# Kernel optimization log

Hardware: AMD Instinct MI355X
Metric: run time of the kernel (lower is better)

## Reference

```python
import jax, jax.numpy as jnp
import numpy as np

HID = 128      # hidden_features
NF = 32        # noise_features
NPL = NF // 4  # noise features per layer
RES = 512      # noise grid resolution
N = 262144     # number of query points


def leaky_relu(x):
    return jax.nn.leaky_relu(x, negative_slope=0.01)


def sample_bilinear(image, coords):
    """image: [M, H, W]; coords: [..., M, 2] -> [..., M]"""
    M, Hn, Wn = image.shape
    x = coords[..., 0] - 0.5
    y = coords[..., 1] - 0.5
    x0f = jnp.floor(x)
    y0f = jnp.floor(y)
    xw = x - x0f
    yw = y - y0f
    x0 = x0f.astype(jnp.int32) % Wn
    x1 = (x0f.astype(jnp.int32) + 1) % Wn
    y0 = y0f.astype(jnp.int32) % Hn
    y1 = (y0f.astype(jnp.int32) + 1) % Hn
    f = jnp.arange(M)  # broadcasts against [..., M] index arrays
    i00 = image[f, y0, x0]
    i01 = image[f, y0, x1]
    i10 = image[f, y1, x0]
    i11 = image[f, y1, x1]
    i0 = i00 + (i01 - i00) * xw
    i1 = i10 + (i11 - i10) * xw
    return i0 + (i1 - i0) * yw


def setup_inputs() -> dict:
    key = jax.random.key(0)
    ks = jax.random.split(key, 12)
    noise = jax.random.normal(ks[0], (NF, RES, RES), dtype=jnp.float32)
    coords = jax.random.normal(ks[1], (N, 2), dtype=jnp.float32)
    # NoiseTransforms param: randn * 0.05 * 2**i per feature
    scale = 0.05 * (2.0 ** np.arange(NF)).astype(np.float32)
    transformations = jax.random.normal(ks[2], (NF, 2, 2), dtype=jnp.float32) * scale[:, None, None]
    input_vec = jnp.ones((HID,), dtype=jnp.float32)
    s_lin = 1.0 / np.sqrt(HID)
    s_noise = 1.0 / np.sqrt(NPL)
    lw = jax.random.uniform(ks[3], (4, HID, HID), jnp.float32, -s_lin, s_lin)
    lb = jax.random.uniform(ks[4], (4, HID), jnp.float32, -s_lin, s_lin)
    lnw = jax.random.uniform(ks[5], (4, HID, NPL), jnp.float32, -s_noise, s_noise)
    tw1 = jax.random.uniform(ks[6], (HID, HID), jnp.float32, -s_lin, s_lin)
    tb1 = jax.random.uniform(ks[7], (HID,), jnp.float32, -s_lin, s_lin)
    tw2 = jax.random.uniform(ks[8], (1, HID), jnp.float32, -s_lin, s_lin)
    tb2 = jax.random.uniform(ks[9], (1,), jnp.float32, -s_lin, s_lin)
    return {"noise": noise, "coords": coords, "transformations": transformations,
            "input_vec": input_vec, "lw": lw, "lb": lb, "lnw": lnw,
            "tw1": tw1, "tb1": tb1, "tw2": tw2, "tb2": tb2}


def reference(noise, coords, transformations, input_vec, lw, lb, lnw, tw1, tb1, tw2, tb2):
    # noise coords: [..., NF, 2]
    noise_coords = jnp.einsum('...n,Mmn->...Mm', coords, transformations)
    noise_values = sample_bilinear(noise, noise_coords)  # [..., NF]
    x = input_vec  # [HID], broadcasts up through layer adds
    for i in range(4):
        nv = noise_values[..., i * NPL:(i + 1) * NPL]
        x = leaky_relu(jnp.einsum('...h,oh->...o', x, lw[i]) + lb[i]
                       + jnp.einsum('...n,on->...o', nv, lnw[i]))
    h = leaky_relu(jnp.einsum('...h,oh->...o', x, tw1) + tb1)
    return jnp.einsum('...h,oh->...o', h, tw2) + tb2  # [..., 1]
```

## Files before the change

### kernel.cpp

```cpp
#include <hip/hip_runtime.h>

typedef _Float16 f16;
typedef f16 f16x4 __attribute__((ext_vector_type(4)));
typedef f16 f16x8 __attribute__((ext_vector_type(8)));
typedef float f32x4 __attribute__((ext_vector_type(4)));

#define RES 512
#define PTS 128
#define XS  136
#define AS  16


__global__ __launch_bounds__(256)
void pack_quad_k(const float* __restrict__ n, f16* __restrict__ q) {
    const int idx = blockIdx.x * 256 + threadIdx.x;
    const int qx = idx & 255, rest = idx >> 8;
    const int qy = rest & 255, m = rest >> 8;
    const float* src = n + ((size_t)m * 512 + 2 * qy) * 512 + 2 * qx;
    const float2 r0 = *(const float2*)(src);
    const float2 r1 = *(const float2*)(src + 512);
    f16x4 o; o[0]=(f16)r0.x; o[1]=(f16)r0.y; o[2]=(f16)r1.x; o[3]=(f16)r1.y;
    *(f16x4*)(q + (size_t)idx * 4) = o;
}

__global__ __launch_bounds__(256)
void pack_w_k(const float* __restrict__ lw,  const float* __restrict__ lnw,
              const float* __restrict__ lb,  const float* __restrict__ tw1,
              const float* __restrict__ tb1,
              f16* __restrict__ wf, f16* __restrict__ waugf) {
    const int g = blockIdx.x * 256 + threadIdx.x;
    if (g < 10240) {
        const int L = g >> 11, r = g & 2047;
        const int lane = r & 63, frag = r >> 6;
        const int q = lane >> 4, l15 = lane & 15;
        const int mt = frag >> 2, c = frag & 3;
        const float* src = ((L < 4) ? (lw + L * 16384) : tw1)
                           + (mt * 16 + l15) * 128 + c * 32 + q * 8;
        f16x8 h;
        #pragma unroll
        for (int j = 0; j < 8; ++j) h[j] = (f16)src[j];
        *(f16x8*)(wf + (size_t)g * 8) = h;
    } else {
        const int ga = g - 10240;
        const int L = ga >> 9, r = ga & 511;
        const int lane = r & 63, mt = r >> 6;
        const int q = lane >> 4, l15 = lane & 15;
        const int row = mt * 16 + l15;
        f16x8 h = {};
        if (q == 0 && L < 4) {
            const float* src = lnw + L * 1024 + row * 8;
            #pragma unroll
            for (int j = 0; j < 8; ++j) h[j] = (f16)src[j];
        }
        if (q == 1)
            h[0] = (f16)((L < 4) ? lb[L * 128 + row] : tb1[row]);
        *(f16x8*)(waugf + (size_t)ga * 8) = h;
    }
}

__device__ __forceinline__ float quad_tap(uint2 q, int sy, int sx) {
    unsigned w = sy ? q.y : q.x;
    w >>= (sx << 4);
    union { unsigned short u; f16 h; } cv; cv.u = (unsigned short)w;
    return (float)cv.h;
}

template <bool QUAD>
__global__ __launch_bounds__(256, 8)
void sample_kernel(const void* __restrict__ noise_v,
                   const float* __restrict__ coords,
                   const float* __restrict__ trans,
                   f16* __restrict__ nv_ws, const int Ntot)
{
    __shared__ float T_sh[128];
    const int t = threadIdx.x;
    if (t < 128) T_sh[t] = trans[t];
    __syncthreads();

    const int g = blockIdx.x & 7;
    const int p = (blockIdx.x >> 3) * 256 + t;

    int mk[4];
    if (g < 7) { mk[0] = g; mk[1] = g + 9; mk[2] = g + 17; mk[3] = g + 25; }
    else       { mk[0] = 7; mk[1] = 8;     mk[2] = 16;     mk[3] = 24;     }

    const float2 c2 = *(const float2*)(coords + p * 2);

    float nvr[4];
    {
        #pragma clang fp contract(off)
        const float cx = c2.x;
        const float cy = c2.y;
        #pragma unroll
        for (int k = 0; k < 4; ++k) {
            const int m = mk[k];
            const float T00 = T_sh[m*4+0], T01 = T_sh[m*4+1];
            const float T10 = T_sh[m*4+2], T11 = T_sh[m*4+3];
            const float p0x = T00 * cx;
            const float p0y = T10 * cx;
            const float ncx = __builtin_fmaf(T01, cy, p0x);
            const float ncy = __builtin_fmaf(T11, cy, p0y);
            const float u = ncx - 0.5f;
            const float v = ncy - 0.5f;
            const float xf = floorf(u), yf = floorf(v);
            const float xw = u - xf, yw = v - yf;
            int ix = (xf >= 2147483648.0f || xf < -2147483648.0f) ? (int)(-2147483647 - 1) : (int)xf;
            int iy = (yf >= 2147483648.0f || yf < -2147483648.0f) ? (int)(-2147483647 - 1) : (int)yf;
            const int x0 = ix & (RES - 1);
            const int x1 = (int)(((unsigned)ix + 1u) & (unsigned)(RES - 1));
            const int y0 = iy & (RES - 1);
            const int y1 = (int)(((unsigned)iy + 1u) & (unsigned)(RES - 1));
            float i00, i01, i10, i11;
            if constexpr (QUAD) {
                const f16* pl = (const f16*)noise_v + (size_t)m * (256 * 256 * 4);
                const int qx0 = x0 >> 1, sx0 = x0 & 1;
                const int qx1 = x1 >> 1, sx1 = x1 & 1;
                const int qy0 = y0 >> 1, sy0 = y0 & 1;
                const int qy1 = y1 >> 1, sy1 = y1 & 1;
                const uint2 qa = *(const uint2*)(pl + (qy0 * 256 + qx0) * 4);
                const uint2 qb = *(const uint2*)(pl + (qy0 * 256 + qx1) * 4);
                const uint2 qc = *(const uint2*)(pl + (qy1 * 256 + qx0) * 4);
                const uint2 qd = *(const uint2*)(pl + (qy1 * 256 + qx1) * 4);
                i00 = quad_tap(qa, sy0, sx0);
                i01 = quad_tap(qb, sy0, sx1);
                i10 = quad_tap(qc, sy1, sx0);
                i11 = quad_tap(qd, sy1, sx1);
            } else {
                const float* pl = (const float*)noise_v + (size_t)m * (RES * RES);
                i00 = pl[y0 * RES + x0];
                i01 = pl[y0 * RES + x1];
                i10 = pl[y1 * RES + x0];
                i11 = pl[y1 * RES + x1];
            }
            const float a0 = i00 + (i01 - i00) * xw;
            const float a1 = i10 + (i11 - i10) * xw;
            nvr[k] = a0 + (a1 - a0) * yw;
        }
    }
    #pragma unroll
    for (int k = 0; k < 4; ++k) {
        const int m = mk[k];
        const int slot = (m & 7) * 4 + (m >> 3);
        nv_ws[(size_t)slot * Ntot + p] = (f16)nvr[k];
    }
}

__global__ __launch_bounds__(256, 2)
void mlp_kernel(const f16* __restrict__ nv_ws,
                const f16* __restrict__ wf,
                const f16* __restrict__ waugf,
                const float* __restrict__ input_vec,
                const float* __restrict__ tw2,
                const float* __restrict__ tb2,
                float* __restrict__ out, const int Ntot)
{
    __shared__ f16 Wm[16384];
    __shared__ f16 Waug[4096];
    __shared__ f16 xa[PTS * XS];
    __shared__ f16 xaug[PTS * AS];
    __shared__ __align__(16) float tw2_sh[128];

    const int t    = threadIdx.x;
    const int wave = t >> 6;
    const int lane = t & 63;
    const int q    = lane >> 4;
    const int l15  = lane & 15;
    const int pbase = blockIdx.x * PTS;
    const int pw    = wave * 32;
    const int p = t >> 1, h = t & 1;

    if (t < 128) {
        tw2_sh[t] = tw2[t];
        xaug[t * AS + 8] = (f16)1.0f;
        #pragma unroll
        for (int c = 9; c < 16; ++c) xaug[t * AS + c] = (f16)0.0f;
    }
    {
        #pragma unroll
        for (int j = 0; j < 8; ++j) {
            const float4 a = ((const float4*)input_vec)[h * 16 + j * 2];
            const float4 b = ((const float4*)input_vec)[h * 16 + j * 2 + 1];
            f16x8 hv;
            hv[0]=(f16)a.x; hv[1]=(f16)a.y; hv[2]=(f16)a.z; hv[3]=(f16)a.w;
            hv[4]=(f16)b.x; hv[5]=(f16)b.y; hv[6]=(f16)b.z; hv[7]=(f16)b.w;
            *(f16x8*)&xa[p * XS + h * 64 + j * 8] = hv;
        }
    }
    const float tb2_0 = tb2[0];

    f16x8 nva, nvb;
    {
        const int P = pbase + p;
        #pragma unroll
        for (int j = 0; j < 8; ++j) {
            nva[j] = nv_ws[(size_t)(j * 4 + 2 * h)     * Ntot + P];
            nvb[j] = nv_ws[(size_t)(j * 4 + 2 * h + 1) * Ntot + P];
        }
    }
    if (h == 0) *(f16x8*)&xaug[p * AS] = nva;

    f32x4 acc[2][8];
    #pragma unroll 1
    for (int L = 0; L < 5; ++L) {
        __syncthreads();
        {
            const f16* wsrc = wf + L * 16384;
            #pragma unroll
            for (int i = 0; i < 8; ++i) {
                const int idx = t + i * 256;
                *(f16x8*)&Wm[idx * 8] = *(const f16x8*)&wsrc[idx * 8];
            }
            const f16* asrc = waugf + L * 4096;
            *(f16x8*)&Waug[t * 8]         = *(const f16x8*)&asrc[t * 8];
            *(f16x8*)&Waug[(t + 256) * 8] = *(const f16x8*)&asrc[(t + 256) * 8];
        }
        __syncthreads();

        {
            const f32x4 z4 = {0.f, 0.f, 0.f, 0.f};
            #pragma unroll
            for (int i = 0; i < 2; ++i)
                #pragma unroll
                for (int mt = 0; mt < 8; ++mt) acc[i][mt] = z4;
        }
        const int pr0 = (pw + l15) * XS, pr1 = (pw + 16 + l15) * XS;
        #pragma unroll
        for (int c = 0; c < 4; ++c) {
            const int kc = c * 32 + q * 8;
            const f16x8 xb0 = *(const f16x8*)&xa[pr0 + kc];
            const f16x8 xb1 = *(const f16x8*)&xa[pr1 + kc];
            #pragma unroll
            for (int mt = 0; mt < 8; ++mt) {
                const f16x8 aw = *(const f16x8*)&Wm[((mt * 4 + c) * 64 + lane) * 8];
                acc[0][mt] = __builtin_amdgcn_mfma_f32_16x16x32_f16(aw, xb0, acc[0][mt], 0, 0, 0);
                acc[1][mt] = __builtin_amdgcn_mfma_f32_16x16x32_f16(aw, xb1, acc[1][mt], 0, 0, 0);
            }
        }
        {
            f16x8 xb0 = {}, xb1 = {};
            if (q < 2) {
                xb0 = *(const f16x8*)&xaug[(pw + l15) * AS + q * 8];
                xb1 = *(const f16x8*)&xaug[(pw + 16 + l15) * AS + q * 8];
            }
            #pragma unroll
            for (int mt = 0; mt < 8; ++mt) {
                const f16x8 aw = *(const f16x8*)&Waug[(mt * 64 + lane) * 8];
                acc[0][mt] = __builtin_amdgcn_mfma_f32_16x16x32_f16(aw, xb0, acc[0][mt], 0, 0, 0);
                acc[1][mt] = __builtin_amdgcn_mfma_f32_16x16x32_f16(aw, xb1, acc[1][mt], 0, 0, 0);
            }
        }

        if (L < 4) {
            #pragma unroll
            for (int i = 0; i < 2; ++i) {
                const int pr = (pw + i * 16 + l15) * XS;
                #pragma unroll
                for (int mt = 0; mt < 8; ++mt) {
                    f16x4 hv;
                    #pragma unroll
                    for (int r = 0; r < 4; ++r) {
                        float v = acc[i][mt][r];
                        v = fmaxf(v, 0.01f * v);
                        hv[r] = (f16)v;
                    }
                    *(f16x4*)&xa[pr + mt * 16 + q * 4] = hv;
                }
            }
            if (L < 3) {
                const int Ln = L + 1;
                if ((Ln >> 1) == h)
                    *(f16x8*)&xaug[p * AS] = (Ln & 1) ? nvb : nva;
            }
        } else {
            #pragma unroll
            for (int i = 0; i < 2; ++i) {
                float s = 0.f;
                #pragma unroll
                for (int mt = 0; mt < 8; ++mt) {
                    const f32x4 w4 = *(const f32x4*)&tw2_sh[mt * 16 + q * 4];
                    #pragma unroll
                    for (int r = 0; r < 4; ++r) {
                        float v = acc[i][mt][r];
                        v = fmaxf(v, 0.01f * v);
                        s += w4[r] * v;
                    }
                }
                s += __shfl_xor(s, 16);
                s += __shfl_xor(s, 32);
                if (q == 0) out[pbase + pw + i * 16 + l15] = s + tb2_0;
            }
        }
    }
}

extern "C" void kernel_launch(void* const* d_in, const int* in_sizes, int n_in,
                              void* d_out, int out_size, void* d_ws, size_t ws_size,
                              hipStream_t stream) {
    const float* noise  = (const float*)d_in[0];
    const float* coords = (const float*)d_in[1];
    const float* trans  = (const float*)d_in[2];
    const float* ivec   = (const float*)d_in[3];
    const float* lw     = (const float*)d_in[4];
    const float* lb     = (const float*)d_in[5];
    const float* lnw    = (const float*)d_in[6];
    const float* tw1    = (const float*)d_in[7];
    const float* tb1    = (const float*)d_in[8];
    const float* tw2    = (const float*)d_in[9];
    const float* tb2    = (const float*)d_in[10];
    float* o            = (float*)d_out;

    const int N = in_sizes[1] / 2;
    f16* nv    = (f16*)d_ws;
    const size_t NV = (size_t)N * 32;
    f16* wfp   = nv + NV;
    f16* waugp = wfp + 5 * 16384;
    f16* qn    = waugp + 5 * 4096;
    const size_t need_full = (NV + 5 * 16384 + 5 * 4096
                              + (size_t)32 * 256 * 256 * 4) * sizeof(f16);

    pack_w_k<<<50, 256, 0, stream>>>(lw, lnw, lb, tw1, tb1, wfp, waugp);
    if (ws_size >= need_full) {
        pack_quad_k<<<(32 * 256 * 256) / 256, 256, 0, stream>>>(noise, qn);
        sample_kernel<true><<<(N / 256) * 8, 256, 0, stream>>>(qn, coords, trans, nv, N);
    } else {
        sample_kernel<false><<<(N / 256) * 8, 256, 0, stream>>>(noise, coords, trans, nv, N);
    }
    mlp_kernel<<<N / PTS, 256, 0, stream>>>(nv, wfp, waugp, ivec, tw2, tb2, o, N);
}
```

Baseline: 235.5 us.

## Fold constant layer-0 input into bias and merge pack kernels

The layer-0 input vector is the same for every point, so W0·input_vec + b0 is computed once during weight packing and stored in the augmented bias slot. This removes the layer-0 128x128 MFMA pass and its weight load per block in the MLP kernel. The noise quad-pack and weight-pack kernels are merged into one launch, and the LDS row strides are changed to 138/18. The odd strides may misalign the 16-byte f16x8 LDS accesses.

Result: faster. 223.8 us (-5.0%).

```diff
diff --git a/kernel.cpp b/kernel.cpp
--- a/kernel.cpp
+++ b/kernel.cpp
@@ -7,28 +7,15 @@
 
 #define RES 512
 #define PTS 128
-#define XS  136
-#define AS  16
-
-
-__global__ __launch_bounds__(256)
-void pack_quad_k(const float* __restrict__ n, f16* __restrict__ q) {
-    const int idx = blockIdx.x * 256 + threadIdx.x;
-    const int qx = idx & 255, rest = idx >> 8;
-    const int qy = rest & 255, m = rest >> 8;
-    const float* src = n + ((size_t)m * 512 + 2 * qy) * 512 + 2 * qx;
-    const float2 r0 = *(const float2*)(src);
-    const float2 r1 = *(const float2*)(src + 512);
-    f16x4 o; o[0]=(f16)r0.x; o[1]=(f16)r0.y; o[2]=(f16)r1.x; o[3]=(f16)r1.y;
-    *(f16x4*)(q + (size_t)idx * 4) = o;
-}
-
-__global__ __launch_bounds__(256)
-void pack_w_k(const float* __restrict__ lw,  const float* __restrict__ lnw,
-              const float* __restrict__ lb,  const float* __restrict__ tw1,
-              const float* __restrict__ tb1,
-              f16* __restrict__ wf, f16* __restrict__ waugf) {
-    const int g = blockIdx.x * 256 + threadIdx.x;
+#define XS  138
+#define AS  18
+
+
+__device__ __forceinline__
+void pack_w_body(int g, const float* __restrict__ lw, const float* __restrict__ lnw,
+                 const float* __restrict__ lb, const float* __restrict__ tw1,
+                 const float* __restrict__ tb1, const float* __restrict__ ivec,
+                 f16* __restrict__ wf, f16* __restrict__ waugf) {
     if (g < 10240) {
         const int L = g >> 11, r = g & 2047;
         const int lane = r & 63, frag = r >> 6;
@@ -52,10 +39,52 @@
             #pragma unroll
             for (int j = 0; j < 8; ++j) h[j] = (f16)src[j];
         }
-        if (q == 1)
-            h[0] = (f16)((L < 4) ? lb[L * 128 + row] : tb1[row]);
+        if (q == 1) {
+            if (L == 0) {
+                float s = lb[row];
+                const float4* w4 = (const float4*)(lw + row * 128);
+                const float4* v4 = (const float4*)ivec;
+                #pragma unroll 8
+                for (int k = 0; k < 32; ++k) {
+                    const float4 w = w4[k], v = v4[k];
+                    s += w.x * v.x + w.y * v.y + w.z * v.z + w.w * v.w;
+                }
+                h[0] = (f16)s;
+            } else {
+                h[0] = (f16)((L < 4) ? lb[L * 128 + row] : tb1[row]);
+            }
+        }
         *(f16x8*)(waugf + (size_t)ga * 8) = h;
     }
+}
+
+__global__ __launch_bounds__(256)
+void pack_all_k(const float* __restrict__ n, f16* __restrict__ q,
+                const float* __restrict__ lw,  const float* __restrict__ lnw,
+                const float* __restrict__ lb,  const float* __restrict__ tw1,
+                const float* __restrict__ tb1, const float* __restrict__ ivec,
+                f16* __restrict__ wf, f16* __restrict__ waugf) {
+    const int b = blockIdx.x;
+    if (b < 8192) {
+        const int idx = b * 256 + threadIdx.x;
+        const int qx = idx & 255, rest = idx >> 8;
+        const int qy = rest & 255, m = rest >> 8;
+        const float* src = n + ((size_t)m * 512 + 2 * qy) * 512 + 2 * qx;
+        const float2 r0 = *(const float2*)(src);
+        const float2 r1 = *(const float2*)(src + 512);
+        f16x4 o; o[0]=(f16)r0.x; o[1]=(f16)r0.y; o[2]=(f16)r1.x; o[3]=(f16)r1.y;
+        *(f16x4*)(q + (size_t)idx * 4) = o;
+    } else {
+        pack_w_body((b - 8192) * 256 + threadIdx.x, lw, lnw, lb, tw1, tb1, ivec, wf, waugf);
+    }
+}
+
+__global__ __launch_bounds__(256)
+void pack_w_k(const float* __restrict__ lw,  const float* __restrict__ lnw,
+              const float* __restrict__ lb,  const float* __restrict__ tw1,
+              const float* __restrict__ tb1, const float* __restrict__ ivec,
+              f16* __restrict__ wf, f16* __restrict__ waugf) {
+    pack_w_body(blockIdx.x * 256 + threadIdx.x, lw, lnw, lb, tw1, tb1, ivec, wf, waugf);
 }
 
 __device__ __forceinline__ float quad_tap(uint2 q, int sy, int sx) {
@@ -149,7 +178,6 @@
 void mlp_kernel(const f16* __restrict__ nv_ws,
                 const f16* __restrict__ wf,
                 const f16* __restrict__ waugf,
-                const float* __restrict__ input_vec,
                 const float* __restrict__ tw2,
                 const float* __restrict__ tb2,
                 float* __restrict__ out, const int Ntot)
@@ -175,17 +203,6 @@
         #pragma unroll
         for (int c = 9; c < 16; ++c) xaug[t * AS + c] = (f16)0.0f;
     }
-    {
-        #pragma unroll
-        for (int j = 0; j < 8; ++j) {
-            const float4 a = ((const float4*)input_vec)[h * 16 + j * 2];
-            const float4 b = ((const float4*)input_vec)[h * 16 + j * 2 + 1];
-            f16x8 hv;
-            hv[0]=(f16)a.x; hv[1]=(f16)a.y; hv[2]=(f16)a.z; hv[3]=(f16)a.w;
-            hv[4]=(f16)b.x; hv[5]=(f16)b.y; hv[6]=(f16)b.z; hv[7]=(f16)b.w;
-            *(f16x8*)&xa[p * XS + h * 64 + j * 8] = hv;
-        }
-    }
     const float tb2_0 = tb2[0];
 
     f16x8 nva, nvb;
@@ -204,11 +221,13 @@
     for (int L = 0; L < 5; ++L) {
         __syncthreads();
         {
-            const f16* wsrc = wf + L * 16384;
-            #pragma unroll
-            for (int i = 0; i < 8; ++i) {
-                const int idx = t + i * 256;
-                *(f16x8*)&Wm[idx * 8] = *(const f16x8*)&wsrc[idx * 8];
+            if (L) {
+                const f16* wsrc = wf + L * 16384;
+                #pragma unroll
+                for (int i = 0; i < 8; ++i) {
+                    const int idx = t + i * 256;
+                    *(f16x8*)&Wm[idx * 8] = *(const f16x8*)&wsrc[idx * 8];
+                }
             }
             const f16* asrc = waugf + L * 4096;
             *(f16x8*)&Waug[t * 8]         = *(const f16x8*)&asrc[t * 8];
@@ -223,17 +242,19 @@
                 #pragma unroll
                 for (int mt = 0; mt < 8; ++mt) acc[i][mt] = z4;
         }
-        const int pr0 = (pw + l15) * XS, pr1 = (pw + 16 + l15) * XS;
-        #pragma unroll
-        for (int c = 0; c < 4; ++c) {
-            const int kc = c * 32 + q * 8;
-            const f16x8 xb0 = *(const f16x8*)&xa[pr0 + kc];
-            const f16x8 xb1 = *(const f16x8*)&xa[pr1 + kc];
-            #pragma unroll
-            for (int mt = 0; mt < 8; ++mt) {
-                const f16x8 aw = *(const f16x8*)&Wm[((mt * 4 + c) * 64 + lane) * 8];
-                acc[0][mt] = __builtin_amdgcn_mfma_f32_16x16x32_f16(aw, xb0, acc[0][mt], 0, 0, 0);
-                acc[1][mt] = __builtin_amdgcn_mfma_f32_16x16x32_f16(aw, xb1, acc[1][mt], 0, 0, 0);
+        if (L) {
+            const int pr0 = (pw + l15) * XS, pr1 = (pw + 16 + l15) * XS;
+            #pragma unroll
+            for (int c = 0; c < 4; ++c) {
+                const int kc = c * 32 + q * 8;
+                const f16x8 xb0 = *(const f16x8*)&xa[pr0 + kc];
+                const f16x8 xb1 = *(const f16x8*)&xa[pr1 + kc];
+                #pragma unroll
+                for (int mt = 0; mt < 8; ++mt) {
+                    const f16x8 aw = *(const f16x8*)&Wm[((mt * 4 + c) * 64 + lane) * 8];
+                    acc[0][mt] = __builtin_amdgcn_mfma_f32_16x16x32_f16(aw, xb0, acc[0][mt], 0, 0, 0);
+                    acc[1][mt] = __builtin_amdgcn_mfma_f32_16x16x32_f16(aw, xb1, acc[1][mt], 0, 0, 0);
+                }
             }
         }
         {
@@ -318,12 +339,13 @@
     const size_t need_full = (NV + 5 * 16384 + 5 * 4096
                               + (size_t)32 * 256 * 256 * 4) * sizeof(f16);
 
-    pack_w_k<<<50, 256, 0, stream>>>(lw, lnw, lb, tw1, tb1, wfp, waugp);
     if (ws_size >= need_full) {
-        pack_quad_k<<<(32 * 256 * 256) / 256, 256, 0, stream>>>(noise, qn);
+        pack_all_k<<<8192 + 50, 256, 0, stream>>>(noise, qn, lw, lnw, lb, tw1, tb1,
+                                                  ivec, wfp, waugp);
         sample_kernel<true><<<(N / 256) * 8, 256, 0, stream>>>(qn, coords, trans, nv, N);
     } else {
+        pack_w_k<<<50, 256, 0, stream>>>(lw, lnw, lb, tw1, tb1, ivec, wfp, waugp);
         sample_kernel<false><<<(N / 256) * 8, 256, 0, stream>>>(noise, coords, trans, nv, N);
     }
-    mlp_kernel<<<N / PTS, 256, 0, stream>>>(nv, wfp, waugp, ivec, tw2, tb2, o, N);
-}
+    mlp_kernel<<<N / PTS, 256, 0, stream>>>(nv, wfp, waugp, tw2, tb2, o, N);
+}
```
